# Kernel tuning notes

Hardware: AMD Instinct MI355X
Metric: run time of the kernel (lower is better)

Reference implementation:

```python
import jax, jax.numpy as jnp
import numpy as np

SEQ, BS, DIM = 2048, 2, 256
G, NQ = 2, 8           # n_keys groups, n_queries total
SUB = NQ // G          # queries per group
EPS = 1e-5


def _ln(x, gamma, beta):
    m = jnp.mean(x, axis=-1, keepdims=True)
    v = jnp.mean(jnp.square(x - m), axis=-1, keepdims=True)
    return (x - m) * jax.lax.rsqrt(v + EPS) * gamma + beta


def setup_inputs() -> dict:
    key = jax.random.key(0)
    ks = jax.random.split(key, 16)
    s = 0.02
    return {
        "x":   jax.random.normal(ks[0], (SEQ, BS, DIM), jnp.float32),
        # block layernorms
        "g0": jnp.ones((DIM,), jnp.float32), "b0": jnp.zeros((DIM,), jnp.float32),
        "g1": jnp.ones((DIM,), jnp.float32), "b1": jnp.zeros((DIM,), jnp.float32),
        # attention q/k layernorm (norm_kvs=True)
        "gn": jnp.ones((DIM,), jnp.float32), "bn": jnp.zeros((DIM,), jnp.float32),
        # attention projections (torch Linear: weight [out,in])
        "wk": jax.random.normal(ks[1], (DIM * G, DIM), jnp.float32) * s,
        "bk": jnp.zeros((DIM * G,), jnp.float32),
        "wv": jax.random.normal(ks[2], (DIM * G, DIM), jnp.float32) * s,
        "bv": jnp.zeros((DIM * G,), jnp.float32),
        "wq": jax.random.normal(ks[3], (DIM * NQ, DIM), jnp.float32) * s,
        "bq": jnp.zeros((DIM * NQ,), jnp.float32),
        "wo": jax.random.normal(ks[4], (DIM, DIM * NQ), jnp.float32) * s,
        "bo": jnp.zeros((DIM,), jnp.float32),
        # FFN: BayesLora(dim,2dim) -> relu -> BayesLora(2dim,dim), eval == plain linear
        "w1": jax.random.normal(ks[5], (2 * DIM, DIM), jnp.float32) * s,
        "bf1": jnp.zeros((2 * DIM,), jnp.float32),
        "w2": jax.random.normal(ks[6], (DIM, 2 * DIM), jnp.float32) * s,
        "bf2": jnp.zeros((DIM,), jnp.float32),
    }


def reference(x, g0, b0, g1, b1, gn, bn, wk, bk, wv, bv, wq, bq, wo, bo, w1, bf1, w2, bf2):
    seq, bs, dim = x.shape
    # --- attention (pre-norm) ---
    h = _ln(x, g0, b0)                                        # s b d
    K = (h @ wk.T + bk).reshape(seq, bs, G, dim)              # s b g i
    V = (h @ wv.T + bv).reshape(seq, bs, G, dim)              # s b g i
    Q = (h @ wq.T + bq).reshape(seq, bs, G, SUB, dim)         # s b g u i
    K = _ln(K, gn, bn)
    Q = _ln(Q, gn, bn)
    scores = jnp.einsum('sbgui,tbgi->bgust', Q, K) / jnp.sqrt(jnp.float32(dim))
    neg = jnp.finfo(scores.dtype).min
    causal = jnp.tril(jnp.ones((seq, seq), bool))             # s1 >= s2 allowed
    scores = jnp.where(causal, scores, neg)
    probs = jax.nn.softmax(scores, axis=-1)                   # b g u s t
    out = jnp.einsum('bgust,tbgi->sbgui', probs, V)
    out = out.reshape(seq, bs, G * SUB * dim)                 # s b (g u i)
    x = x + (out @ wo.T + bo)
    # --- FFN (pre-norm) ---
    h2 = _ln(x, g1, b1)
    f = jax.nn.relu(h2 @ w1.T + bf1) @ w2.T + bf2
    return x + f
```

## Files before the change

kernel.cpp:

```cpp
#include <hip/hip_runtime.h>
#include <hip/hip_bf16.h>

#define SEQ  2048
#define BSZ  2
#define DIM  256
#define NG   2
#define NQH  8
#define SUBQ 4
#define ROWS (SEQ*BSZ)
#define NQKV 3072
#define QROW 6144

typedef unsigned int uint32;
typedef unsigned short ushort;
typedef __attribute__((ext_vector_type(8))) short short8;
typedef __attribute__((ext_vector_type(4))) float f32x4;

__device__ __forceinline__ float bflo(uint32 u){
  union { uint32 i; float f; } c; c.i = u << 16; return c.f;
}
__device__ __forceinline__ float bfhi(uint32 u){
  union { uint32 i; float f; } c; c.i = u & 0xffff0000u; return c.f;
}
__device__ __forceinline__ uint32 pack2(float a, float b){
  __hip_bfloat16 ha = __float2bfloat16(a);
  __hip_bfloat16 hb = __float2bfloat16(b);
  unsigned short ua, ub;
  __builtin_memcpy(&ua, &ha, 2);
  __builtin_memcpy(&ub, &hb, 2);
  return (uint32)ua | ((uint32)ub << 16);
}
__device__ __forceinline__ ushort bf16bits(float v){
  __hip_bfloat16 h = __float2bfloat16(v);
  ushort u; __builtin_memcpy(&u, &h, 2); return u;
}

__device__ __forceinline__ void dma16(const void* g, void* l) {
  __builtin_amdgcn_global_load_lds(
      (const __attribute__((address_space(1))) uint32*)g,
      (__attribute__((address_space(3))) uint32*)l, 16, 0, 0);
}

__global__ __launch_bounds__(256) void misc0(
    const float* __restrict__ wk, const float* __restrict__ wv,
    const float* __restrict__ wq, const float* __restrict__ wo,
    const float* __restrict__ w1, const float* __restrict__ w2,
    const float* __restrict__ bk, const float* __restrict__ bv,
    const float* __restrict__ bq,
    __hip_bfloat16* __restrict__ out, float* __restrict__ bc,
    const float* __restrict__ x, const float* __restrict__ g0,
    const float* __restrict__ b0, __hip_bfloat16* __restrict__ Hf)
{
  if (blockIdx.x < 771) {
    int u = blockIdx.x * 256 + threadIdx.x;
    if (u < 196608) {
      int lane = u & 63, col = lane & 15, quad = lane >> 4;
      const float* srcrow;
      if (u < 98304) {
        int n16 = u >> 9, kc = (u >> 6) & 7;
        int n = n16 * 16 + col;
        const float* m = (n < 512) ? (wk + (size_t)n * 256)
                       : (n < 1024) ? (wv + (size_t)(n - 512) * 256)
                                    : (wq + (size_t)(n - 1024) * 256);
        srcrow = m + kc * 32 + quad * 8;
      } else if (u < 163840) {
        int local = u - 98304;
        int n16 = local >> 12, kc = (local >> 6) & 63;
        srcrow = wo + (size_t)(n16 * 16 + col) * 2048 + kc * 32 + quad * 8;
      } else if (u < 180224) {
        int local = u - 163840;
        int n16 = local >> 9, kc = (local >> 6) & 7;
        srcrow = w1 + (size_t)(n16 * 16 + col) * 256 + kc * 32 + quad * 8;
      } else {
        int local = u - 180224;
        int n16 = local >> 10, kc = (local >> 6) & 15;
        srcrow = w2 + (size_t)(n16 * 16 + col) * 512 + kc * 32 + quad * 8;
      }
      float4 a = *(const float4*)srcrow;
      float4 b = *(const float4*)(srcrow + 4);
      uint4 st;
      st.x = pack2(a.x, a.y); st.y = pack2(a.z, a.w);
      st.z = pack2(b.x, b.y); st.w = pack2(b.z, b.w);
      *(uint4*)((ushort*)out + (size_t)u * 8) = st;
    } else {
      int bu = u - 196608;
      const float* src; int loc;
      if      (bu < 128) { src = bk; loc = bu; }
      else if (bu < 256) { src = bv; loc = bu - 128; }
      else               { src = bq; loc = bu - 256; }
      *(float4*)(bc + 4 * (size_t)bu) = *(const float4*)(src + 4 * (size_t)loc);
    }
  } else {
    int wave = threadIdx.x >> 6, lane = threadIdx.x & 63;
    int row = (blockIdx.x - 771) * 4 + wave;
    size_t base = (size_t)row * DIM + lane * 4;
    float4 v = *(const float4*)(x + base);
    float s  = v.x + v.y + v.z + v.w;
    float s2 = v.x*v.x + v.y*v.y + v.z*v.z + v.w*v.w;
    #pragma unroll
    for (int o = 1; o < 64; o <<= 1) {
      s  += __shfl_xor(s, o);
      s2 += __shfl_xor(s2, o);
    }
    float m = s * (1.0f / DIM);
    float rb = rsqrtf(s2 * (1.0f / DIM) - m * m + 1e-5f);
    float4 gm = *(const float4*)(g0 + lane * 4);
    float4 bt = *(const float4*)(b0 + lane * 4);
    uint2 st;
    st.x = pack2((v.x - m) * rb * gm.x + bt.x, (v.y - m) * rb * gm.y + bt.y);
    st.y = pack2((v.z - m) * rb * gm.z + bt.z, (v.w - m) * rb * gm.w + bt.w);
    int kc = lane >> 3, quad = (lane >> 1) & 3, jj = 4 * (lane & 1);
    int cid = (row >> 4) * 8 + kc;
    *(uint2*)((ushort*)Hf + (size_t)cid * 512 + (quad * 16 + (row & 15)) * 8 + jj) = st;
  }
}

__global__ __launch_bounds__(256) void ln_swz(
    __hip_bfloat16* __restrict__ QKV,
    const float* __restrict__ gamma, const float* __restrict__ beta,
    __hip_bfloat16* __restrict__ Kf, __hip_bfloat16* __restrict__ Vf)
{
  int j = blockIdx.x;
  if (j < 10240) {
    int wave = threadIdx.x >> 6, lane = threadIdx.x & 63;
    int idx = j * 4 + wave;
    size_t base;
    if (idx < 8192) base = (size_t)(idx >> 1) * NQKV + (idx & 1) * DIM;
    else {
      int qi = idx - 8192;
      base = (size_t)(qi >> 3) * NQKV + 2 * NG * DIM + (qi & 7) * DIM;
    }
    __hip_bfloat16* p = QKV + base + lane * 4;
    uint2 u = *(const uint2*)p;
    float v0 = bflo(u.x), v1 = bfhi(u.x), v2 = bflo(u.y), v3 = bfhi(u.y);
    float s  = v0 + v1 + v2 + v3;
    float s2 = v0*v0 + v1*v1 + v2*v2 + v3*v3;
    #pragma unroll
    for (int o = 1; o < 64; o <<= 1) {
      s  += __shfl_xor(s, o);
      s2 += __shfl_xor(s2, o);
    }
    float m = s * (1.0f / DIM);
    float rb = rsqrtf(s2 * (1.0f / DIM) - m * m + 1e-5f);
    float4 gm = *(const float4*)(gamma + lane * 4);
    float4 bt = *(const float4*)(beta + lane * 4);
    uint2 st;
    st.x = pack2((v0 - m) * rb * gm.x + bt.x, (v1 - m) * rb * gm.y + bt.y);
    st.y = pack2((v2 - m) * rb * gm.z + bt.z, (v3 - m) * rb * gm.w + bt.w);
    if (idx < 8192) {
      int r = idx >> 1, gg = idx & 1;
      int t = r >> 1, b = r & 1;
      int bg = b * NG + gg;
      int kt = t >> 5, tr = t & 31, tc = tr >> 4, col = tr & 15;
      int ks = lane >> 3, quad = (lane >> 1) & 3, jj = 4 * (lane & 1);
      int cid = (bg * 64 + kt) * 16 + tc * 8 + ks;
      *(uint2*)((ushort*)Kf + (size_t)cid * 512 + (quad * 16 + col) * 8 + jj) = st;
    } else {
      *(uint2*)p = st;
    }
  } else {
    __shared__ ushort T[64][72];
    int vb = j - 10240;
    int t0 = (vb & 31) * 64, d0 = ((vb >> 5) & 3) * 64, bg = vb >> 7;
    int b = bg >> 1, g = bg & 1;
    int tid = threadIdx.x;
    int tr = tid >> 2, c4 = (tid & 3) * 16;
    const ushort* src = (const ushort*)QKV + ((size_t)(t0 + tr) * BSZ + b) * NQKV
                      + NG * DIM + g * DIM + d0 + c4;
    uint4 a0 = *(const uint4*)src;
    uint4 a1 = *(const uint4*)(src + 8);
    *(uint4*)&T[tr][c4]     = a0;
    *(uint4*)&T[tr][c4 + 8] = a1;
    __syncthreads();
    #pragma unroll
    for (int k2 = 0; k2 < 2; ++k2) {
      int u = tid * 2 + k2;
      int tt = u >> 8, di = (u >> 6) & 3, qd = (u >> 4) & 3, cl = u & 15;
      ushort tmp[8];
      #pragma unroll
      for (int e = 0; e < 8; ++e) tmp[e] = T[tt * 32 + qd * 8 + e][di * 16 + cl];
      int kt = (t0 >> 5) + tt;
      int dc = (d0 >> 4) + di;
      *(uint4*)((ushort*)Vf + (((size_t)(bg * 64 + kt) * 16 + dc) << 9) + (qd * 16 + cl) * 8)
          = *(uint4*)tmp;
    }
  }
}

template<int GN, int RELU, int OUTMODE, int AFRAG>
__global__ __launch_bounds__(256) void gemm_mfma(
    const __hip_bfloat16* __restrict__ A,
    const __hip_bfloat16* __restrict__ W,
    const float* __restrict__ bias,
    const float* __restrict__ resid,
    void* __restrict__ outp,
    int M, int N, int K)
{
  constexpr int WCH = GN / 16;
  constexpr int MC  = (GN == 128) ? 4 : 2;
  __shared__ __align__(16) ushort AS[2][4096];
  __shared__ __align__(16) ushort WS[2][WCH * 512];

  const int tid = threadIdx.x;
  const int wave = tid >> 6, lane = tid & 63;
  const int col = lane & 15, quad = lane >> 4;
  const int wm = (GN == 128) ? (wave >> 1) : wave;
  const int wn = (GN == 128) ? (wave & 1) : 0;
  const int bn0 = blockIdx.x * GN;
  const int bm0 = blockIdx.y * 128;
  const int Keff  = (OUTMODE == 2) ? (K / gridDim.z) : K;
  const int kbase = (OUTMODE == 2) ? blockIdx.z * Keff : 0;
  const int kiters = Keff >> 5;

  f32x4 acc[MC][4];
  #pragma unroll
  for (int mc = 0; mc < MC; ++mc)
    #pragma unroll
    for (int nc = 0; nc < 4; ++nc)
      acc[mc][nc] = (f32x4){0.f, 0.f, 0.f, 0.f};

  auto stage = [&](int it, int bufi) {
    int k0 = kbase + it * 32;
    #pragma unroll
    for (int c = 0; c < 2; ++c) {
      int ch = wave * 2 + c;
      if (AFRAG)
        dma16((const ushort*)A + ((((size_t)(bm0 >> 4) + ch) * (K >> 5) + (k0 >> 5)) << 9) + lane * 8,
              &AS[bufi][ch * 512]);
      else
        dma16((const ushort*)A + (size_t)(bm0 + ch * 16 + col) * K + k0 + quad * 8,
              &AS[bufi][ch * 512]);
    }
    #pragma unroll
    for (int c = 0; c < WCH / 4; ++c) {
      int ch = wave * (WCH / 4) + c;
      dma16((const ushort*)W + (((size_t)((bn0 >> 4) + ch) * (K >> 5) + (k0 >> 5)) << 9) + lane * 8,
            &WS[bufi][ch * 512]);
    }
  };

  stage(0, 0);
  for (int it = 0; it < kiters; ++it) {
    int cur = it & 1;
    __syncthreads();
    if (it + 1 < kiters) stage(it + 1, 1 - cur);
    short8 af[MC], bf_[4];
    #pragma unroll
    for (int mc = 0; mc < MC; ++mc)
      af[mc] = *(const short8*)&AS[cur][(wm * MC + mc) * 512 + lane * 8];
    #pragma unroll
    for (int nc = 0; nc < 4; ++nc)
      bf_[nc] = *(const short8*)&WS[cur][(wn * 4 + nc) * 512 + lane * 8];
    #pragma unroll
    for (int mc = 0; mc < MC; ++mc)
      #pragma unroll
      for (int nc = 0; nc < 4; ++nc)
        acc[mc][nc] = __builtin_amdgcn_mfma_f32_16x16x32_bf16(af[mc], bf_[nc], acc[mc][nc], 0, 0, 0);
  }

  #pragma unroll
  for (int nc = 0; nc < 4; ++nc) {
    int n = bn0 + wn * 64 + nc * 16 + col;
    float bv = 0.f;
    if (OUTMODE != 2) bv = bias[n];
    #pragma unroll
    for (int mc = 0; mc < MC; ++mc) {
      #pragma unroll
      for (int reg = 0; reg < 4; ++reg) {
        int m = bm0 + wm * (MC * 16) + mc * 16 + quad * 4 + reg;
        float v = acc[mc][nc][reg] + bv;
        if (OUTMODE != 2 && resid) v += resid[(size_t)m * N + n];
        if (RELU) v = fmaxf(v, 0.f);
        if (OUTMODE == 0)
          ((__hip_bfloat16*)outp)[(size_t)m * N + n] = __float2bfloat16(v);
        else if (OUTMODE == 1)
          ((float*)outp)[(size_t)m * N + n] = v;
        else
          ((float*)outp)[(size_t)blockIdx.z * M * N + (size_t)m * N + n] = v;
      }
    }
  }
}

__global__ __launch_bounds__(256) void combine2(
    const float* __restrict__ P, const float* __restrict__ bias,
    const float* __restrict__ resid, float* __restrict__ out, int MN)
{
  int i4 = (blockIdx.x * 256 + threadIdx.x) * 4;
  float4 a = *(const float4*)(P + i4);
  float4 b = *(const float4*)(P + MN + i4);
  float4 r = *(const float4*)(resid + i4);
  float4 bb = *(const float4*)(bias + (i4 & (DIM - 1)));
  float4 o;
  o.x = a.x + b.x + r.x + bb.x;
  o.y = a.y + b.y + r.y + bb.y;
  o.z = a.z + b.z + r.z + bb.z;
  o.w = a.w + b.w + r.w + bb.w;
  *(float4*)(out + i4) = o;
}

__global__ __launch_bounds__(256) void combine_ln4(
    const float* __restrict__ P, const float* __restrict__ bias,
    const float* __restrict__ resid, float* __restrict__ X2,
    const float* __restrict__ gamma, const float* __restrict__ beta,
    __hip_bfloat16* __restrict__ H2f)
{
  const int MN = ROWS * DIM;
  int wave = threadIdx.x >> 6, lane = threadIdx.x & 63;
  int row = blockIdx.x * 4 + wave;
  size_t i = (size_t)row * DIM + lane * 4;
  float4 a = *(const float4*)(P + i);
  float4 b = *(const float4*)(P + MN + i);
  float4 c = *(const float4*)(P + 2 * (size_t)MN + i);
  float4 d = *(const float4*)(P + 3 * (size_t)MN + i);
  float4 r = *(const float4*)(resid + i);
  float4 bb = *(const float4*)(bias + lane * 4);
  float4 v;
  v.x = a.x + b.x + c.x + d.x + r.x + bb.x;
  v.y = a.y + b.y + c.y + d.y + r.y + bb.y;
  v.z = a.z + b.z + c.z + d.z + r.z + bb.z;
  v.w = a.w + b.w + c.w + d.w + r.w + bb.w;
  *(float4*)(X2 + i) = v;
  float s  = v.x + v.y + v.z + v.w;
  float s2 = v.x*v.x + v.y*v.y + v.z*v.z + v.w*v.w;
  #pragma unroll
  for (int o = 1; o < 64; o <<= 1) {
    s  += __shfl_xor(s, o);
    s2 += __shfl_xor(s2, o);
  }
  float m = s * (1.0f / DIM);
  float rb = rsqrtf(s2 * (1.0f / DIM) - m * m + 1e-5f);
  float4 gm = *(const float4*)(gamma + lane * 4);
  float4 bt = *(const float4*)(beta + lane * 4);
  uint2 st;
  st.x = pack2((v.x - m) * rb * gm.x + bt.x, (v.y - m) * rb * gm.y + bt.y);
  st.y = pack2((v.z - m) * rb * gm.z + bt.z, (v.w - m) * rb * gm.w + bt.w);
  int kc = lane >> 3, quad = (lane >> 1) & 3, jj = 4 * (lane & 1);
  int cid = (row >> 4) * 8 + kc;
  *(uint2*)((ushort*)H2f + (size_t)cid * 512 + (quad * 16 + (row & 15)) * 8 + jj) = st;
}

__global__ __launch_bounds__(256, 2) void attn_mfma(
    const __hip_bfloat16* __restrict__ QKV,
    const __hip_bfloat16* __restrict__ Kf,
    const __hip_bfloat16* __restrict__ Vf,
    __hip_bfloat16* __restrict__ Ob,
    __hip_bfloat16* __restrict__ Op1,
    float* __restrict__ Lp)
{
  __shared__ __align__(16) ushort KS[2][8192];
  __shared__ __align__(16) ushort VS[2][8192];
  __shared__ __align__(16) ushort Pw[4][1280];

  const int tid  = threadIdx.x;
  const int wave = tid >> 6, lane = tid & 63;
  const int col  = lane & 15, quad = lane >> 4;
  const int head = blockIdx.x & 15;
  const int w    = blockIdx.x >> 4;
  int qb, z, split, nit, k0;
  if (w < 24) { qb = 15 - (w >> 1); z = w & 1; split = 1; nit = 2 * qb + 2; k0 = z * nit; }
  else        { qb = 27 - w;        z = 0;     split = 0; nit = 4 * qb + 4; k0 = 0; }

  const int b = head >> 3, hq = head & 7, g = hq >> 2;
  const int bg = b * NG + g;
  const int qw0 = qb * 128 + wave * 32;

  short8 qf[2][8];
  #pragma unroll
  for (int mc = 0; mc < 2; ++mc) {
    int s = qw0 + mc * 16 + col;
    const ushort* qp = (const ushort*)QKV + (size_t)s * QROW + b * NQKV
                     + 2 * NG * DIM + hq * DIM + quad * 8;
    #pragma unroll
    for (int ks = 0; ks < 8; ++ks)
      qf[mc][ks] = *(const short8*)(qp + ks * 32);
  }

  short8 onesf;
  #pragma unroll
  for (int i = 0; i < 8; ++i) onesf[i] = (short)0x3F80;

  f32x4 o[2][16];
  #pragma unroll
  for (int mc = 0; mc < 2; ++mc)
    #pragma unroll
    for (int dc = 0; dc < 16; ++dc)
      o[mc][dc] = (f32x4){0.f, 0.f, 0.f, 0.f};
  float l_s[2][4] = {{0.f}};

  auto stage = [&](int i, int bufi) {
    int kt = k0 + i;
    const ushort* kb = (const ushort*)Kf + (((size_t)bg * 64 + kt) << 13);
    const ushort* vb = (const ushort*)Vf + (((size_t)bg * 64 + kt) << 13);
    #pragma unroll
    for (int cc = 0; cc < 4; ++cc) {
      int nk = wave * 4 + cc;
      dma16(kb + (nk << 9) + lane * 8, &KS[bufi][nk * 512]);
      dma16(vb + (nk << 9) + lane * 8, &VS[bufi][nk * 512]);
    }
  };

  stage(0, 0);
  for (int i = 0; i < nit; ++i) {
    int cur = i & 1;
    __syncthreads();
    if (i + 1 < nit) stage(i + 1, 1 - cur);
    int kt = k0 + i;
    if (kt * 32 > qw0 + 31) continue;

    f32x4 sf[2][2];
    #pragma unroll
    for (int mc = 0; mc < 2; ++mc)
      #pragma unroll
      for (int tc = 0; tc < 2; ++tc)
        sf[mc][tc] = (f32x4){0.f, 0.f, 0.f, 0.f};
    #pragma unroll
    for (int ks = 0; ks < 8; ++ks) {
      short8 kb0 = *(const short8*)&KS[cur][ks * 512 + lane * 8];
      short8 kb1 = *(const short8*)&KS[cur][(8 + ks) * 512 + lane * 8];
      sf[0][0] = __builtin_amdgcn_mfma_f32_16x16x32_bf16(qf[0][ks], kb0, sf[0][0], 0, 0, 0);
      sf[0][1] = __builtin_amdgcn_mfma_f32_16x16x32_bf16(qf[0][ks], kb1, sf[0][1], 0, 0, 0);
      sf[1][0] = __builtin_amdgcn_mfma_f32_16x16x32_bf16(qf[1][ks], kb0, sf[1][0], 0, 0, 0);
      sf[1][1] = __builtin_amdgcn_mfma_f32_16x16x32_bf16(qf[1][ks], kb1, sf[1][1], 0, 0, 0);
    }

    const bool dm = (kt * 32 + 31) > qw0;
    #pragma unroll
    for (int mc = 0; mc < 2; ++mc)
      #pragma unroll
      for (int tc = 0; tc < 2; ++tc)
        #pragma unroll
        for (int reg = 0; reg < 4; ++reg) {
          float p = __expf(sf[mc][tc][reg] * 0.0625f);
          if (dm) {
            int tg = kt * 32 + tc * 16 + col;
            int sg = qw0 + mc * 16 + quad * 4 + reg;
            if (tg > sg) p = 0.f;
          }
          Pw[wave][(mc * 16 + quad * 4 + reg) * 40 + tc * 16 + col] = bf16bits(p);
        }

    short8 pa0 = *(const short8*)&Pw[wave][col * 40 + quad * 8];
    short8 pa1 = *(const short8*)&Pw[wave][(16 + col) * 40 + quad * 8];

    f32x4 zz = (f32x4){0.f, 0.f, 0.f, 0.f};
    f32x4 ps0 = __builtin_amdgcn_mfma_f32_16x16x32_bf16(pa0, onesf, zz, 0, 0, 0);
    f32x4 ps1 = __builtin_amdgcn_mfma_f32_16x16x32_bf16(pa1, onesf, zz, 0, 0, 0);
    #pragma unroll
    for (int r = 0; r < 4; ++r) { l_s[0][r] += ps0[r]; l_s[1][r] += ps1[r]; }

    #pragma unroll
    for (int dc = 0; dc < 16; ++dc) {
      short8 vb = *(const short8*)&VS[cur][dc * 512 + lane * 8];
      o[0][dc] = __builtin_amdgcn_mfma_f32_16x16x32_bf16(pa0, vb, o[0][dc], 0, 0, 0);
      o[1][dc] = __builtin_amdgcn_mfma_f32_16x16x32_bf16(pa1, vb, o[1][dc], 0, 0, 0);
    }
  }

  if (!split) {
    #pragma unroll
    for (int mc = 0; mc < 2; ++mc)
      #pragma unroll
      for (int reg = 0; reg < 4; ++reg) {
        float inv = 1.0f / l_s[mc][reg];
        int s = qw0 + mc * 16 + quad * 4 + reg;
        __hip_bfloat16* op = Ob + (size_t)s * (BSZ * NQH * DIM) + b * (NQH * DIM) + hq * DIM;
        #pragma unroll
        for (int dc = 0; dc < 16; ++dc)
          op[dc * 16 + col] = __float2bfloat16(o[mc][dc][reg] * inv);
      }
  } else {
    #pragma unroll
    for (int mc = 0; mc < 2; ++mc)
      #pragma unroll
      for (int reg = 0; reg < 4; ++reg) {
        int s = qw0 + mc * 16 + quad * 4 + reg;
        int row = s - 512;
        __hip_bfloat16* op = (z == 0)
            ? Ob  + (size_t)s   * (BSZ * NQH * DIM) + b * (NQH * DIM) + hq * DIM
            : Op1 + (size_t)row * (BSZ * NQH * DIM) + b * (NQH * DIM) + hq * DIM;
        #pragma unroll
        for (int dc = 0; dc < 16; ++dc)
          op[dc * 16 + col] = __float2bfloat16(o[mc][dc][reg]);
        if (col == 0) Lp[(z * 1536 + row) * 16 + head] = l_s[mc][reg];
      }
  }
}

__global__ __launch_bounds__(256) void attn_norm(
    __hip_bfloat16* __restrict__ Ob, const __hip_bfloat16* __restrict__ Op1,
    const float* __restrict__ Lp)
{
  int i4 = (blockIdx.x * 256 + threadIdx.x) * 4;
  int row = i4 >> 12;
  int off = i4 & 4095;
  int head = off >> 8;
  float inv = 1.0f / (Lp[row * 16 + head] + Lp[(1536 + row) * 16 + head]);
  ushort* a = (ushort*)Ob + (size_t)(row + 512) * 4096 + off;
  const ushort* c = (const ushort*)Op1 + (size_t)row * 4096 + off;
  uint2 ua = *(const uint2*)a;
  uint2 uc = *(const uint2*)c;
  uint2 st;
  st.x = pack2((bflo(ua.x) + bflo(uc.x)) * inv, (bfhi(ua.x) + bfhi(uc.x)) * inv);
  st.y = pack2((bflo(ua.y) + bflo(uc.y)) * inv, (bfhi(ua.y) + bfhi(uc.y)) * inv);
  *(uint2*)a = st;
}

extern "C" void kernel_launch(void* const* d_in, const int* in_sizes, int n_in,
                              void* d_out, int out_size, void* d_ws, size_t ws_size,
                              hipStream_t stream)
{
  const float* x   = (const float*)d_in[0];
  const float* g0  = (const float*)d_in[1];
  const float* b0  = (const float*)d_in[2];
  const float* g1  = (const float*)d_in[3];
  const float* b1  = (const float*)d_in[4];
  const float* gn  = (const float*)d_in[5];
  const float* bn  = (const float*)d_in[6];
  const float* wk  = (const float*)d_in[7];
  const float* bk  = (const float*)d_in[8];
  const float* wv  = (const float*)d_in[9];
  const float* bv  = (const float*)d_in[10];
  const float* wq  = (const float*)d_in[11];
  const float* bq  = (const float*)d_in[12];
  const float* wo  = (const float*)d_in[13];
  const float* bo  = (const float*)d_in[14];
  const float* w1  = (const float*)d_in[15];
  const float* bf1 = (const float*)d_in[16];
  const float* w2  = (const float*)d_in[17];
  const float* bf2 = (const float*)d_in[18];

  char* ws = (char*)d_ws;
  const size_t MB = 1024 * 1024;
  __hip_bfloat16* QKV = (__hip_bfloat16*)(ws);
  float*          Pwo = (float*)         (ws);
  float*          X2  = (float*)         (ws + 16 * MB);
  __hip_bfloat16* H2f = (__hip_bfloat16*)(ws + 20 * MB);
  __hip_bfloat16* F1  = (__hip_bfloat16*)(ws + 22 * MB);
  __hip_bfloat16* Hf  = (__hip_bfloat16*)(ws + 24 * MB);
  __hip_bfloat16* Kf  = (__hip_bfloat16*)(ws + 24 * MB);
  __hip_bfloat16* Vf  = (__hip_bfloat16*)(ws + 28 * MB);
  __hip_bfloat16* AO  = (__hip_bfloat16*)(ws + 32 * MB);
  __hip_bfloat16* Op1 = (__hip_bfloat16*)(ws + 48 * MB);
  float*          Pw2 = (float*)         (ws + 48 * MB);
  float*          BC  = (float*)         (ws + 60 * MB + 768 * 1024);
  float*          Lp  = (float*)         (ws + 60 * MB + 800 * 1024);
  __hip_bfloat16* WB  = (__hip_bfloat16*)(ws + 61 * MB);

  __hip_bfloat16* woB = WB + 786432;
  __hip_bfloat16* w1B = WB + 1310720;
  __hip_bfloat16* w2B = WB + 1441792;

  misc0<<<1795, 256, 0, stream>>>(wk, wv, wq, wo, w1, w2, bk, bv, bq, WB, BC, x, g0, b0, Hf);
  gemm_mfma<128,0,0,1><<<dim3(NQKV/128, ROWS/128), 256, 0, stream>>>(Hf, WB, BC, nullptr, QKV, ROWS, NQKV, DIM);
  ln_swz<<<12288, 256, 0, stream>>>(QKV, gn, bn, Kf, Vf);
  attn_mfma<<<448, 256, 0, stream>>>(QKV, Kf, Vf, AO, Op1, Lp);
  attn_norm<<<6144, 256, 0, stream>>>(AO, Op1, Lp);
  gemm_mfma<64,0,2,0><<<dim3(DIM/64, ROWS/128, 4), 256, 0, stream>>>(AO, woB, nullptr, nullptr, Pwo, ROWS, DIM, NQH*DIM);
  combine_ln4<<<ROWS / 4, 256, 0, stream>>>(Pwo, bo, x, X2, g1, b1, H2f);
  gemm_mfma<64,1,0,1><<<dim3((2*DIM)/64, ROWS/128), 256, 0, stream>>>(H2f, w1B, bf1, nullptr, F1, ROWS, 2*DIM, DIM);
  gemm_mfma<64,0,2,0><<<dim3(DIM/64, ROWS/128, 2), 256, 0, stream>>>(F1, w2B, nullptr, nullptr, Pw2, ROWS, DIM, 2*DIM);
  combine2<<<ROWS*DIM/1024, 256, 0, stream>>>(Pw2, bf2, X2, (float*)d_out, ROWS*DIM);
}
```

Before: 249.3 us.

## Write attention and FFN outputs in MFMA fragment layout and store split-K partials as bf16

The attention kernel and the FFN1 GEMM now write their outputs directly in the swizzled fragment layout that the next GEMM loads with AFRAG. This replaces the strided row-major A loads. Split-K partial sums for the wo and w2 GEMMs are stored as bf16 instead of fp32, which halves the partial-buffer traffic read by the combine kernels. attn_norm now works on 8-element fragment chunks. The bf16 partials lose some precision in the residual sums.

After: 248.8 us. No clear change (-0.2%).

```diff
diff --git a/kernel.cpp b/kernel.cpp
--- a/kernel.cpp
+++ b/kernel.cpp
@@ -208,8 +208,9 @@
   const int wn = (GN == 128) ? (wave & 1) : 0;
   const int bn0 = blockIdx.x * GN;
   const int bm0 = blockIdx.y * 128;
-  const int Keff  = (OUTMODE == 2) ? (K / gridDim.z) : K;
-  const int kbase = (OUTMODE == 2) ? blockIdx.z * Keff : 0;
+  const bool SPLIT = (OUTMODE == 2 || OUTMODE == 4);
+  const int Keff  = SPLIT ? (K / gridDim.z) : K;
+  const int kbase = SPLIT ? blockIdx.z * Keff : 0;
   const int kiters = Keff >> 5;
 
   f32x4 acc[MC][4];
@@ -262,45 +263,53 @@
   for (int nc = 0; nc < 4; ++nc) {
     int n = bn0 + wn * 64 + nc * 16 + col;
     float bv = 0.f;
-    if (OUTMODE != 2) bv = bias[n];
+    if (OUTMODE == 0 || OUTMODE == 1 || OUTMODE == 3) bv = bias[n];
     #pragma unroll
     for (int mc = 0; mc < MC; ++mc) {
       #pragma unroll
       for (int reg = 0; reg < 4; ++reg) {
         int m = bm0 + wm * (MC * 16) + mc * 16 + quad * 4 + reg;
         float v = acc[mc][nc][reg] + bv;
-        if (OUTMODE != 2 && resid) v += resid[(size_t)m * N + n];
+        if ((OUTMODE == 0 || OUTMODE == 1 || OUTMODE == 3) && resid)
+          v += resid[(size_t)m * N + n];
         if (RELU) v = fmaxf(v, 0.f);
         if (OUTMODE == 0)
           ((__hip_bfloat16*)outp)[(size_t)m * N + n] = __float2bfloat16(v);
         else if (OUTMODE == 1)
           ((float*)outp)[(size_t)m * N + n] = v;
-        else
+        else if (OUTMODE == 2)
           ((float*)outp)[(size_t)blockIdx.z * M * N + (size_t)m * N + n] = v;
+        else if (OUTMODE == 3) {
+          int cid = (m >> 4) * (N >> 5) + (n >> 5);
+          int kl = n & 31;
+          ((ushort*)outp)[(size_t)cid * 512 + ((kl >> 3) * 16 + (m & 15)) * 8 + (kl & 7)] = bf16bits(v);
+        } else {
+          ((ushort*)outp)[(size_t)blockIdx.z * M * N + (size_t)m * N + n] = bf16bits(v);
+        }
       }
     }
   }
 }
 
 __global__ __launch_bounds__(256) void combine2(
-    const float* __restrict__ P, const float* __restrict__ bias,
+    const ushort* __restrict__ P, const float* __restrict__ bias,
     const float* __restrict__ resid, float* __restrict__ out, int MN)
 {
   int i4 = (blockIdx.x * 256 + threadIdx.x) * 4;
-  float4 a = *(const float4*)(P + i4);
-  float4 b = *(const float4*)(P + MN + i4);
+  uint2 a = *(const uint2*)(P + i4);
+  uint2 b = *(const uint2*)(P + MN + i4);
   float4 r = *(const float4*)(resid + i4);
   float4 bb = *(const float4*)(bias + (i4 & (DIM - 1)));
   float4 o;
-  o.x = a.x + b.x + r.x + bb.x;
-  o.y = a.y + b.y + r.y + bb.y;
-  o.z = a.z + b.z + r.z + bb.z;
-  o.w = a.w + b.w + r.w + bb.w;
+  o.x = bflo(a.x) + bflo(b.x) + r.x + bb.x;
+  o.y = bfhi(a.x) + bfhi(b.x) + r.y + bb.y;
+  o.z = bflo(a.y) + bflo(b.y) + r.z + bb.z;
+  o.w = bfhi(a.y) + bfhi(b.y) + r.w + bb.w;
   *(float4*)(out + i4) = o;
 }
 
 __global__ __launch_bounds__(256) void combine_ln4(
-    const float* __restrict__ P, const float* __restrict__ bias,
+    const ushort* __restrict__ P, const float* __restrict__ bias,
     const float* __restrict__ resid, float* __restrict__ X2,
     const float* __restrict__ gamma, const float* __restrict__ beta,
     __hip_bfloat16* __restrict__ H2f)
@@ -309,17 +318,17 @@
   int wave = threadIdx.x >> 6, lane = threadIdx.x & 63;
   int row = blockIdx.x * 4 + wave;
   size_t i = (size_t)row * DIM + lane * 4;
-  float4 a = *(const float4*)(P + i);
-  float4 b = *(const float4*)(P + MN + i);
-  float4 c = *(const float4*)(P + 2 * (size_t)MN + i);
-  float4 d = *(const float4*)(P + 3 * (size_t)MN + i);
+  uint2 a = *(const uint2*)(P + i);
+  uint2 b = *(const uint2*)(P + MN + i);
+  uint2 c = *(const uint2*)(P + 2 * (size_t)MN + i);
+  uint2 d = *(const uint2*)(P + 3 * (size_t)MN + i);
   float4 r = *(const float4*)(resid + i);
   float4 bb = *(const float4*)(bias + lane * 4);
   float4 v;
-  v.x = a.x + b.x + c.x + d.x + r.x + bb.x;
-  v.y = a.y + b.y + c.y + d.y + r.y + bb.y;
-  v.z = a.z + b.z + c.z + d.z + r.z + bb.z;
-  v.w = a.w + b.w + c.w + d.w + r.w + bb.w;
+  v.x = bflo(a.x) + bflo(b.x) + bflo(c.x) + bflo(d.x) + r.x + bb.x;
+  v.y = bfhi(a.x) + bfhi(b.x) + bfhi(c.x) + bfhi(d.x) + r.y + bb.y;
+  v.z = bflo(a.y) + bflo(b.y) + bflo(c.y) + bflo(d.y) + r.z + bb.z;
+  v.w = bfhi(a.y) + bfhi(b.y) + bfhi(c.y) + bfhi(d.y) + r.w + bb.w;
   *(float4*)(X2 + i) = v;
   float s  = v.x + v.y + v.z + v.w;
   float s2 = v.x*v.x + v.y*v.y + v.z*v.z + v.w*v.w;
@@ -344,8 +353,8 @@
     const __hip_bfloat16* __restrict__ QKV,
     const __hip_bfloat16* __restrict__ Kf,
     const __hip_bfloat16* __restrict__ Vf,
-    __hip_bfloat16* __restrict__ Ob,
-    __hip_bfloat16* __restrict__ Op1,
+    __hip_bfloat16* __restrict__ Obf,
+    __hip_bfloat16* __restrict__ Op1f,
     float* __restrict__ Lp)
 {
   __shared__ __align__(16) ushort KS[2][8192];
@@ -457,53 +466,64 @@
     }
   }
 
-  if (!split) {
-    #pragma unroll
-    for (int mc = 0; mc < 2; ++mc)
-      #pragma unroll
-      for (int reg = 0; reg < 4; ++reg) {
-        float inv = 1.0f / l_s[mc][reg];
-        int s = qw0 + mc * 16 + quad * 4 + reg;
-        __hip_bfloat16* op = Ob + (size_t)s * (BSZ * NQH * DIM) + b * (NQH * DIM) + hq * DIM;
+  const int colh = col >> 3, coll = col & 7;
+  #pragma unroll
+  for (int mc = 0; mc < 2; ++mc)
+    #pragma unroll
+    for (int reg = 0; reg < 4; ++reg) {
+      int s = qw0 + mc * 16 + quad * 4 + reg;
+      int m = s * BSZ + b;
+      int m16 = m >> 4, ml = m & 15;
+      float inv = 1.0f / l_s[mc][reg];
+      if (!split) {
         #pragma unroll
-        for (int dc = 0; dc < 16; ++dc)
-          op[dc * 16 + col] = __float2bfloat16(o[mc][dc][reg] * inv);
+        for (int dc = 0; dc < 16; ++dc) {
+          int cid = m16 * 64 + hq * 8 + (dc >> 1);
+          int qt = (dc & 1) * 2 + colh;
+          Obf[(size_t)cid * 512 + (qt * 16 + ml) * 8 + coll] =
+              __float2bfloat16(o[mc][dc][reg] * inv);
+        }
+      } else {
+        #pragma unroll
+        for (int dc = 0; dc < 16; ++dc) {
+          int qt = (dc & 1) * 2 + colh;
+          size_t off;
+          __hip_bfloat16* dst;
+          if (z == 0) {
+            dst = Obf;  off = ((size_t)(m16 * 64 + hq * 8 + (dc >> 1))) * 512;
+          } else {
+            dst = Op1f; off = ((size_t)((m16 - 64) * 64 + hq * 8 + (dc >> 1))) * 512;
+          }
+          dst[off + (qt * 16 + ml) * 8 + coll] = __float2bfloat16(o[mc][dc][reg]);
+        }
+        if (col == 0) Lp[(z * 1536 + (s - 512)) * 16 + head] = l_s[mc][reg];
       }
-  } else {
-    #pragma unroll
-    for (int mc = 0; mc < 2; ++mc)
-      #pragma unroll
-      for (int reg = 0; reg < 4; ++reg) {
-        int s = qw0 + mc * 16 + quad * 4 + reg;
-        int row = s - 512;
-        __hip_bfloat16* op = (z == 0)
-            ? Ob  + (size_t)s   * (BSZ * NQH * DIM) + b * (NQH * DIM) + hq * DIM
-            : Op1 + (size_t)row * (BSZ * NQH * DIM) + b * (NQH * DIM) + hq * DIM;
-        #pragma unroll
-        for (int dc = 0; dc < 16; ++dc)
-          op[dc * 16 + col] = __float2bfloat16(o[mc][dc][reg]);
-        if (col == 0) Lp[(z * 1536 + row) * 16 + head] = l_s[mc][reg];
-      }
-  }
+    }
 }
 
 __global__ __launch_bounds__(256) void attn_norm(
-    __hip_bfloat16* __restrict__ Ob, const __hip_bfloat16* __restrict__ Op1,
+    __hip_bfloat16* __restrict__ Obf, const __hip_bfloat16* __restrict__ Op1f,
     const float* __restrict__ Lp)
 {
-  int i4 = (blockIdx.x * 256 + threadIdx.x) * 4;
-  int row = i4 >> 12;
-  int off = i4 & 4095;
-  int head = off >> 8;
+  int i8 = blockIdx.x * 256 + threadIdx.x;
+  int cidr = i8 >> 6;
+  int lane = i8 & 63;
+  int m16r = cidr >> 6, kc = cidr & 63;
+  int m = (m16r + 64) * 16 + (lane & 15);
+  int k = kc * 32 + (lane >> 4) * 8;
+  int s = m >> 1, b = m & 1, hq = k >> 8;
+  int row = s - 512, head = b * 8 + hq;
   float inv = 1.0f / (Lp[row * 16 + head] + Lp[(1536 + row) * 16 + head]);
-  ushort* a = (ushort*)Ob + (size_t)(row + 512) * 4096 + off;
-  const ushort* c = (const ushort*)Op1 + (size_t)row * 4096 + off;
-  uint2 ua = *(const uint2*)a;
-  uint2 uc = *(const uint2*)c;
-  uint2 st;
+  ushort* a = (ushort*)Obf + (((size_t)(m16r + 64) * 64 + kc) << 9) + lane * 8;
+  const ushort* c = (const ushort*)Op1f + (((size_t)m16r * 64 + kc) << 9) + lane * 8;
+  uint4 ua = *(const uint4*)a;
+  uint4 uc = *(const uint4*)c;
+  uint4 st;
   st.x = pack2((bflo(ua.x) + bflo(uc.x)) * inv, (bfhi(ua.x) + bfhi(uc.x)) * inv);
   st.y = pack2((bflo(ua.y) + bflo(uc.y)) * inv, (bfhi(ua.y) + bfhi(uc.y)) * inv);
-  *(uint2*)a = st;
+  st.z = pack2((bflo(ua.z) + bflo(uc.z)) * inv, (bfhi(ua.z) + bfhi(uc.z)) * inv);
+  st.w = pack2((bflo(ua.w) + bflo(uc.w)) * inv, (bfhi(ua.w) + bfhi(uc.w)) * inv);
+  *(uint4*)a = st;
 }
 
 extern "C" void kernel_launch(void* const* d_in, const int* in_sizes, int n_in,
@@ -533,16 +553,16 @@
   char* ws = (char*)d_ws;
   const size_t MB = 1024 * 1024;
   __hip_bfloat16* QKV = (__hip_bfloat16*)(ws);
-  float*          Pwo = (float*)         (ws);
+  __hip_bfloat16* Pwo = (__hip_bfloat16*)(ws);
+  __hip_bfloat16* Pw2 = (__hip_bfloat16*)(ws + 8  * MB);
   float*          X2  = (float*)         (ws + 16 * MB);
   __hip_bfloat16* H2f = (__hip_bfloat16*)(ws + 20 * MB);
-  __hip_bfloat16* F1  = (__hip_bfloat16*)(ws + 22 * MB);
+  __hip_bfloat16* F1f = (__hip_bfloat16*)(ws + 22 * MB);
   __hip_bfloat16* Hf  = (__hip_bfloat16*)(ws + 24 * MB);
   __hip_bfloat16* Kf  = (__hip_bfloat16*)(ws + 24 * MB);
   __hip_bfloat16* Vf  = (__hip_bfloat16*)(ws + 28 * MB);
-  __hip_bfloat16* AO  = (__hip_bfloat16*)(ws + 32 * MB);
-  __hip_bfloat16* Op1 = (__hip_bfloat16*)(ws + 48 * MB);
-  float*          Pw2 = (float*)         (ws + 48 * MB);
+  __hip_bfloat16* Obf = (__hip_bfloat16*)(ws + 32 * MB);
+  __hip_bfloat16* Op1f= (__hip_bfloat16*)(ws + 48 * MB);
   float*          BC  = (float*)         (ws + 60 * MB + 768 * 1024);
   float*          Lp  = (float*)         (ws + 60 * MB + 800 * 1024);
   __hip_bfloat16* WB  = (__hip_bfloat16*)(ws + 61 * MB);
@@ -554,11 +574,11 @@
   misc0<<<1795, 256, 0, stream>>>(wk, wv, wq, wo, w1, w2, bk, bv, bq, WB, BC, x, g0, b0, Hf);
   gemm_mfma<128,0,0,1><<<dim3(NQKV/128, ROWS/128), 256, 0, stream>>>(Hf, WB, BC, nullptr, QKV, ROWS, NQKV, DIM);
   ln_swz<<<12288, 256, 0, stream>>>(QKV, gn, bn, Kf, Vf);
-  attn_mfma<<<448, 256, 0, stream>>>(QKV, Kf, Vf, AO, Op1, Lp);
-  attn_norm<<<6144, 256, 0, stream>>>(AO, Op1, Lp);
-  gemm_mfma<64,0,2,0><<<dim3(DIM/64, ROWS/128, 4), 256, 0, stream>>>(AO, woB, nullptr, nullptr, Pwo, ROWS, DIM, NQH*DIM);
-  combine_ln4<<<ROWS / 4, 256, 0, stream>>>(Pwo, bo, x, X2, g1, b1, H2f);
-  gemm_mfma<64,1,0,1><<<dim3((2*DIM)/64, ROWS/128), 256, 0, stream>>>(H2f, w1B, bf1, nullptr, F1, ROWS, 2*DIM, DIM);
-  gemm_mfma<64,0,2,0><<<dim3(DIM/64, ROWS/128, 2), 256, 0, stream>>>(F1, w2B, nullptr, nullptr, Pw2, ROWS, DIM, 2*DIM);
-  combine2<<<ROWS*DIM/1024, 256, 0, stream>>>(Pw2, bf2, X2, (float*)d_out, ROWS*DIM);
-}
+  attn_mfma<<<448, 256, 0, stream>>>(QKV, Kf, Vf, Obf, Op1f, Lp);
+  attn_norm<<<3072, 256, 0, stream>>>(Obf, Op1f, Lp);
+  gemm_mfma<64,0,4,1><<<dim3(DIM/64, ROWS/128, 4), 256, 0, stream>>>(Obf, woB, nullptr, nullptr, Pwo, ROWS, DIM, NQH*DIM);
+  combine_ln4<<<ROWS / 4, 256, 0, stream>>>((const ushort*)Pwo, bo, x, X2, g1, b1, H2f);
+  gemm_mfma<64,1,3,1><<<dim3((2*DIM)/64, ROWS/128), 256, 0, stream>>>(H2f, w1B, bf1, nullptr, F1f, ROWS, 2*DIM, DIM);
+  gemm_mfma<64,0,4,1><<<dim3(DIM/64, ROWS/128, 2), 256, 0, stream>>>(F1f, w2B, nullptr, nullptr, Pw2, ROWS, DIM, 2*DIM);
+  combine2<<<ROWS*DIM/1024, 256, 0, stream>>>((const ushort*)Pw2, bf2, X2, (float*)d_out, ROWS*DIM);
+}
```
